# Kernel tuning notes

Measured on AMD Instinct MI355X. Metric: run time of the kernel, lower is better.

## Reference

```python
import jax, jax.numpy as jnp
from jax import lax
import numpy as np
import math

INPUT_DIM = 64
HIDDEN_DIM = 512
SEQ_LEN = 256
BATCH = 512
PRED_LEN = 24
NUM_TARGETS = 1


def setup_inputs() -> dict:
    key = jax.random.key(0)
    ks = jax.random.split(key, 10)
    stdv = 1.0 / math.sqrt(HIDDEN_DIM)
    u = lambda k, shape: jax.random.uniform(k, shape, jnp.float32, -stdv, stdv)
    return {
        "x": jax.random.normal(ks[0], (BATCH, SEQ_LEN, INPUT_DIM), jnp.float32),
        "Wa": u(ks[1], (INPUT_DIM, INPUT_DIM)),
        "Ua": u(ks[2], (2 * HIDDEN_DIM, INPUT_DIM)),
        "ba": jnp.zeros((INPUT_DIM,), jnp.float32),
        "Va": u(ks[3], (INPUT_DIM, INPUT_DIM)),
        "W_ih": u(ks[4], (4 * HIDDEN_DIM, INPUT_DIM)),
        "W_hh": u(ks[5], (4 * HIDDEN_DIM, HIDDEN_DIM)),
        "b_ih": u(ks[6], (4 * HIDDEN_DIM,)),
        "b_hh": u(ks[7], (4 * HIDDEN_DIM,)),
        "fc_w": u(ks[8], (PRED_LEN * NUM_TARGETS, HIDDEN_DIM)),
        "fc_b": u(ks[9], (PRED_LEN * NUM_TARGETS,)),
    }


def reference(x, Wa, Ua, ba, Va, W_ih, W_hh, b_ih, b_hh, fc_w, fc_b):
    B, S, D = x.shape
    H = W_hh.shape[1]

    def step(carry, x_t):
        h, c = carry  # [B,H] each
        # attention gate over input features
        hc = jnp.concatenate([h, c], axis=1)  # [B,2H]
        a_t = jnp.tanh(x_t @ Wa + hc @ Ua + ba) @ Va  # [B,D]
        alpha_t = jax.nn.softmax(a_t, axis=1)
        x_att = alpha_t * x_t
        # torch.nn.LSTMCell: gates in order i, f, g, o
        gates = x_att @ W_ih.T + h @ W_hh.T + b_ih + b_hh  # [B,4H]
        i, f, g, o = jnp.split(gates, 4, axis=1)
        c_new = jax.nn.sigmoid(f) * c + jax.nn.sigmoid(i) * jnp.tanh(g)
        h_new = jax.nn.sigmoid(o) * jnp.tanh(c_new)
        return (h_new, c_new), None

    h0 = jnp.zeros((B, H), x.dtype)
    c0 = jnp.zeros((B, H), x.dtype)
    (h_T, _), _ = lax.scan(step, (h0, c0), jnp.swapaxes(x, 0, 1))  # scan over seq
    y = h_T @ fc_w.T + fc_b  # [B, pred_len*num_targets]
    return y.reshape(B, PRED_LEN, NUM_TARGETS)
```

## Files before the change

kernel.cpp:

```cpp
#include <hip/hip_runtime.h>
#include <math.h>

#define B 512
#define S 256
#define D 64
#define H 512
#define BH (B*H)

#define HBUF_OFF 0
#define CBUF_OFF (2*BH)
#define XATT_OFF (4*BH)

typedef __attribute__((ext_vector_type(8))) short short8;
typedef __attribute__((ext_vector_type(4))) float f32x4;

__device__ inline unsigned short f2bf(float v) {
    unsigned int u = __float_as_uint(v);
    unsigned int r = (u + 0x7fffu + ((u >> 16) & 1u)) >> 16;
    return (unsigned short)r;
}
__device__ inline float bf2f(unsigned short b) {
    return __uint_as_float(((unsigned int)b) << 16);
}
__device__ inline float readlane_f(float v, int l) {
    return __uint_as_float(__builtin_amdgcn_readlane(__float_as_uint(v), l));
}

__global__ __launch_bounds__(256) void init_zero(float* __restrict__ ws) {
    int i = blockIdx.x * blockDim.x + threadIdx.x;
    if (i < BH) {
        ws[HBUF_OFF + i] = 0.f;
        ws[CBUF_OFF + i] = 0.f;
    }
}

__global__ __launch_bounds__(256) void attn_kernel(
    const float* __restrict__ x, const float* __restrict__ Wa,
    const float* __restrict__ Ua, const float* __restrict__ ba,
    const float* __restrict__ Va, float* __restrict__ ws, int t)
{
    const int tid = threadIdx.x;
    const int lane = tid & 63;
    const int w = tid >> 6;
    const int b0 = blockIdx.x * 4;
    const int rd = t & 1;

    __shared__ float hcx[4][1092];
    __shared__ float part[4][4][64];
    __shared__ float ta4[4][64];

    const float* __restrict__ hbuf = ws + HBUF_OFF + rd*BH;
    const float* __restrict__ cbuf = ws + CBUF_OFF + rd*BH;

    {
        const float4* xs = (const float4*)(x + ((size_t)(b0 + w)*S + t)*D);
        const float4* hs = (const float4*)(hbuf + (size_t)(b0 + w)*H);
        const float4* cs = (const float4*)(cbuf + (size_t)(b0 + w)*H);
        for (int c = lane; c < 272; c += 64) {
            float4 v;
            if (c < 16) v = xs[c];
            else if (c < 144) v = hs[c - 16];
            else v = cs[c - 144];
            *(float4*)&hcx[w][c*4] = v;
        }
    }
    __syncthreads();

    float acc0 = 0.f, acc1 = 0.f, acc2 = 0.f, acc3 = 0.f;
    const int k0 = w * 272;
    for (int kb = 0; kb < 272; kb += 64) {
        const int base = k0 + kb;
        int n = 272 - kb; if (n > 64) n = 64;
        int ii = base + lane; if (ii > 1087) ii = 1087;
        float hv0 = hcx[0][ii];
        float hv1 = hcx[1][ii];
        float hv2 = hcx[2][ii];
        float hv3 = hcx[3][ii];
        #pragma unroll 8
        for (int j = 0; j < n; ++j) {
            const int k = base + j;
            const float* wrow = (k < 64) ? (Wa + k*D) : (Ua + (size_t)(k - 64)*D);
            float uv = wrow[lane];
            acc0 += readlane_f(hv0, j) * uv;
            acc1 += readlane_f(hv1, j) * uv;
            acc2 += readlane_f(hv2, j) * uv;
            acc3 += readlane_f(hv3, j) * uv;
        }
    }
    part[w][0][lane] = acc0;
    part[w][1][lane] = acc1;
    part[w][2][lane] = acc2;
    part[w][3][lane] = acc3;
    __syncthreads();
    {
        float pre = ba[lane] + part[0][w][lane] + part[1][w][lane]
                  + part[2][w][lane] + part[3][w][lane];
        ta4[w][lane] = tanhf(pre);
    }
    __syncthreads();
    {
        float tv = ta4[w][lane];
        float v = 0.f;
        #pragma unroll 8
        for (int j = 0; j < 64; ++j)
            v += readlane_f(tv, j) * Va[j*D + lane];
        float m = v;
        #pragma unroll
        for (int o = 32; o > 0; o >>= 1) m = fmaxf(m, __shfl_xor(m, o));
        float e = expf(v - m);
        float ssum = e;
        #pragma unroll
        for (int o = 32; o > 0; o >>= 1) ssum += __shfl_xor(ssum, o);
        ws[XATT_OFF + (size_t)(b0 + w)*D + lane] = (e / ssum) * hcx[w][lane];
    }
}

__global__ __launch_bounds__(256) void gates_kernel(
    const float* __restrict__ Wih, const float* __restrict__ Whh,
    const float* __restrict__ bih, const float* __restrict__ bhh,
    float* __restrict__ ws, int t)
{
    const int tid = threadIdx.x;
    const int lane = tid & 63;
    const int wid = tid >> 6;
    const int wr = wid >> 1, wc = wid & 1;
    const int ut = blockIdx.x;
    const int rt = blockIdx.y;
    const int b0 = rt * 64;
    const int u_base = ut * 16;

    __shared__ __align__(16) unsigned short aHi[64][72];
    __shared__ __align__(16) unsigned short aLo[64][72];
    __shared__ __align__(16) unsigned short bHi[64][72];
    __shared__ __align__(16) unsigned short bLo[64][72];
    __shared__ float gout[64][66];

    const int rd = t & 1, wrs = rd ^ 1;
    const float* __restrict__ hbuf_r = ws + HBUF_OFF + rd*BH;
    const float* __restrict__ cbuf_r = ws + CBUF_OFF + rd*BH;
    float* __restrict__ hbuf_w = ws + HBUF_OFF + wrs*BH;
    float* __restrict__ cbuf_w = ws + CBUF_OFF + wrs*BH;
    const float* __restrict__ xatt = ws + XATT_OFF;

    const int srow = tid >> 2;
    const int c4 = tid & 3;
    const int Wrow = (srow & 3)*H + u_base + (srow >> 2);

    f32x4 acc00 = {0,0,0,0}, acc01 = {0,0,0,0}, acc10 = {0,0,0,0}, acc11 = {0,0,0,0};
    float4 aReg[4], bReg[4];

    auto loadChunk = [&](int kb) {
        const float* asrc; const float* bsrc;
        if (kb < 8) {
            asrc = hbuf_r + (size_t)(b0 + srow)*H + kb*64;
            bsrc = Whh + (size_t)Wrow*H + kb*64;
        } else {
            asrc = xatt + (size_t)(b0 + srow)*D;
            bsrc = Wih + (size_t)Wrow*D;
        }
        #pragma unroll
        for (int it = 0; it < 4; ++it) {
            const int f = c4 + 4*it;
            aReg[it] = *(const float4*)(asrc + f*4);
            bReg[it] = *(const float4*)(bsrc + f*4);
        }
    };
    auto storeChunk = [&]() {
        #pragma unroll
        for (int it = 0; it < 4; ++it) {
            const int f = c4 + 4*it;
            float4 av = aReg[it], bv = bReg[it];
            ushort4 ah, al, bh, bl;
            ah.x = f2bf(av.x); al.x = f2bf(av.x - bf2f(ah.x));
            ah.y = f2bf(av.y); al.y = f2bf(av.y - bf2f(ah.y));
            ah.z = f2bf(av.z); al.z = f2bf(av.z - bf2f(ah.z));
            ah.w = f2bf(av.w); al.w = f2bf(av.w - bf2f(ah.w));
            bh.x = f2bf(bv.x); bl.x = f2bf(bv.x - bf2f(bh.x));
            bh.y = f2bf(bv.y); bl.y = f2bf(bv.y - bf2f(bh.y));
            bh.z = f2bf(bv.z); bl.z = f2bf(bv.z - bf2f(bh.z));
            bh.w = f2bf(bv.w); bl.w = f2bf(bv.w - bf2f(bh.w));
            *(ushort4*)&aHi[srow][f*4] = ah;
            *(ushort4*)&aLo[srow][f*4] = al;
            *(ushort4*)&bHi[srow][f*4] = bh;
            *(ushort4*)&bLo[srow][f*4] = bl;
        }
    };

    loadChunk(0);
    for (int kb = 0; kb < 9; ++kb) {
        __syncthreads();
        storeChunk();
        __syncthreads();
        if (kb < 8) loadChunk(kb + 1);
        #pragma unroll
        for (int ks = 0; ks < 2; ++ks) {
            const int col = ks*32 + (lane >> 4)*8;
            const int ar0 = wr*32 + (lane & 15);
            const int br0 = wc*32 + (lane & 15);
            short8 ah0 = *(const short8*)&aHi[ar0][col];
            short8 ah1 = *(const short8*)&aHi[ar0 + 16][col];
            short8 al0 = *(const short8*)&aLo[ar0][col];
            short8 al1 = *(const short8*)&aLo[ar0 + 16][col];
            short8 bh0 = *(const short8*)&bHi[br0][col];
            short8 bh1 = *(const short8*)&bHi[br0 + 16][col];
            short8 bl0 = *(const short8*)&bLo[br0][col];
            short8 bl1 = *(const short8*)&bLo[br0 + 16][col];
            acc00 = __builtin_amdgcn_mfma_f32_16x16x32_bf16(ah0, bh0, acc00, 0,0,0);
            acc01 = __builtin_amdgcn_mfma_f32_16x16x32_bf16(ah0, bh1, acc01, 0,0,0);
            acc10 = __builtin_amdgcn_mfma_f32_16x16x32_bf16(ah1, bh0, acc10, 0,0,0);
            acc11 = __builtin_amdgcn_mfma_f32_16x16x32_bf16(ah1, bh1, acc11, 0,0,0);
            acc00 = __builtin_amdgcn_mfma_f32_16x16x32_bf16(ah0, bl0, acc00, 0,0,0);
            acc01 = __builtin_amdgcn_mfma_f32_16x16x32_bf16(ah0, bl1, acc01, 0,0,0);
            acc10 = __builtin_amdgcn_mfma_f32_16x16x32_bf16(ah1, bl0, acc10, 0,0,0);
            acc11 = __builtin_amdgcn_mfma_f32_16x16x32_bf16(ah1, bl1, acc11, 0,0,0);
            acc00 = __builtin_amdgcn_mfma_f32_16x16x32_bf16(al0, bh0, acc00, 0,0,0);
            acc01 = __builtin_amdgcn_mfma_f32_16x16x32_bf16(al0, bh1, acc01, 0,0,0);
            acc10 = __builtin_amdgcn_mfma_f32_16x16x32_bf16(al1, bh0, acc10, 0,0,0);
            acc11 = __builtin_amdgcn_mfma_f32_16x16x32_bf16(al1, bh1, acc11, 0,0,0);
        }
    }

    {
        const int m0 = (lane >> 4)*4;
        const int n0 = lane & 15;
        #pragma unroll
        for (int r = 0; r < 4; ++r) {
            gout[wr*32 + m0 + r     ][wc*32 + n0     ] = acc00[r];
            gout[wr*32 + m0 + r     ][wc*32 + 16 + n0] = acc01[r];
            gout[wr*32 + 16 + m0 + r][wc*32 + n0     ] = acc10[r];
            gout[wr*32 + 16 + m0 + r][wc*32 + 16 + n0] = acc11[r];
        }
    }
    __syncthreads();
    {
        const int u16 = tid & 15;
        const int u_glob = u_base + u16;
        const float bs0 = bih[0*H + u_glob] + bhh[0*H + u_glob];
        const float bs1 = bih[1*H + u_glob] + bhh[1*H + u_glob];
        const float bs2 = bih[2*H + u_glob] + bhh[2*H + u_glob];
        const float bs3 = bih[3*H + u_glob] + bhh[3*H + u_glob];
        #pragma unroll
        for (int pass = 0; pass < 4; ++pass) {
            const int b_loc = (tid >> 4) + pass*16;
            const int b = b0 + b_loc;
            float2 g01 = *(const float2*)&gout[b_loc][u16*4];
            float2 g23 = *(const float2*)&gout[b_loc][u16*4 + 2];
            float gi = g01.x + bs0;
            float gf = g01.y + bs1;
            float gg = g23.x + bs2;
            float go = g23.y + bs3;
            float c_old = cbuf_r[(size_t)b*H + u_glob];
            float si = 1.f/(1.f + expf(-gi));
            float sf = 1.f/(1.f + expf(-gf));
            float so = 1.f/(1.f + expf(-go));
            float cn = sf*c_old + si*tanhf(gg);
            float hn = so*tanhf(cn);
            cbuf_w[(size_t)b*H + u_glob] = cn;
            hbuf_w[(size_t)b*H + u_glob] = hn;
        }
    }
}

__global__ __launch_bounds__(256) void fc_kernel(
    const float* __restrict__ fcw, const float* __restrict__ fcb,
    const float* __restrict__ ws, float* __restrict__ out)
{
    const int b = blockIdx.x;
    __shared__ float hrow[H];
    const float* __restrict__ hp = ws + HBUF_OFF + (size_t)b*H;
    for (int k = threadIdx.x; k < H; k += 256) hrow[k] = hp[k];
    __syncthreads();
    int j = threadIdx.x;
    if (j < 24) {
        float a = fcb[j];
        #pragma unroll 8
        for (int k = 0; k < H; ++k) a += hrow[k] * fcw[j*H + k];
        out[b*24 + j] = a;
    }
}

extern "C" void kernel_launch(void* const* d_in, const int* in_sizes, int n_in,
                              void* d_out, int out_size, void* d_ws, size_t ws_size,
                              hipStream_t stream) {
    const float* x   = (const float*)d_in[0];
    const float* Wa  = (const float*)d_in[1];
    const float* Ua  = (const float*)d_in[2];
    const float* ba  = (const float*)d_in[3];
    const float* Va  = (const float*)d_in[4];
    const float* Wih = (const float*)d_in[5];
    const float* Whh = (const float*)d_in[6];
    const float* bih = (const float*)d_in[7];
    const float* bhh = (const float*)d_in[8];
    const float* fcw = (const float*)d_in[9];
    const float* fcb = (const float*)d_in[10];
    float* out = (float*)d_out;
    float* ws  = (float*)d_ws;

    hipLaunchKernelGGL(init_zero, dim3((BH + 255)/256), dim3(256), 0, stream, ws);
    for (int t = 0; t < S; ++t) {
        hipLaunchKernelGGL(attn_kernel, dim3(B/4), dim3(256), 0, stream,
                           x, Wa, Ua, ba, Va, ws, t);
        hipLaunchKernelGGL(gates_kernel, dim3(32, 8), dim3(256), 0, stream,
                           Wih, Whh, bih, bhh, ws, t);
    }
    hipLaunchKernelGGL(fc_kernel, dim3(B), dim3(256), 0, stream, fcw, fcb, ws, out);
}
```

Baseline: 9.084 ms.

## Pre-split weights into swizzled bf16 hi/lo and double-buffer the gates GEMM

A one-time prep kernel converts W_hh and W_ih into bf16 hi/lo pairs in a swizzled layout, so the gates kernel loads its B fragments straight into registers instead of converting them through LDS at every timestep. The gates kernel also writes h as bf16 hi/lo, and the attention kernel writes x_att the same way, so the A operand is staged into double-buffered LDS with a single barrier per k-chunk. The attention kernel is rewritten to handle two batch rows per block, reading h, c and weights directly from global memory. That rewrite gives up the four-row weight reuse of the old readlane scheme and may cost more in the attention step. The c state now uses one in-place buffer.

```diff
diff --git a/kernel.cpp b/kernel.cpp
--- a/kernel.cpp
+++ b/kernel.cpp
@@ -7,9 +7,6 @@
 #define H 512
 #define BH (B*H)
 
-#define HBUF_OFF 0
-#define CBUF_OFF (2*BH)
-#define XATT_OFF (4*BH)
 
 typedef __attribute__((ext_vector_type(8))) short short8;
 typedef __attribute__((ext_vector_type(4))) float f32x4;
@@ -22,103 +19,125 @@
 __device__ inline float bf2f(unsigned short b) {
     return __uint_as_float(((unsigned int)b) << 16);
 }
-__device__ inline float readlane_f(float v, int l) {
-    return __uint_as_float(__builtin_amdgcn_readlane(__float_as_uint(v), l));
-}
-
-__global__ __launch_bounds__(256) void init_zero(float* __restrict__ ws) {
+
+__global__ __launch_bounds__(256) void init_zero(
+    float* __restrict__ h32, float* __restrict__ c32,
+    unsigned short* __restrict__ hHi, unsigned short* __restrict__ hLo)
+{
     int i = blockIdx.x * blockDim.x + threadIdx.x;
     if (i < BH) {
-        ws[HBUF_OFF + i] = 0.f;
-        ws[CBUF_OFF + i] = 0.f;
+        h32[i] = 0.f;
+        c32[i] = 0.f;
+        hHi[i] = 0;
+        hLo[i] = 0;
+    }
+}
+
+__global__ __launch_bounds__(256) void prep_weights(
+    const float* __restrict__ Whh, const float* __restrict__ Wih,
+    unsigned short* __restrict__ wswz)
+{
+    const int ut = blockIdx.x;
+    const int kb = blockIdx.y;
+    const int t = threadIdx.x;
+    const int srow = t >> 2;
+    const int cc0 = (t & 3) * 16;
+    const int Wrow = (srow & 3)*H + ut*16 + (srow >> 2);
+
+    const float* src = (kb < 8) ? (Whh + (size_t)Wrow*H + kb*64 + cc0)
+                                : (Wih + (size_t)Wrow*D + cc0);
+    float v[16];
+    #pragma unroll
+    for (int i = 0; i < 4; ++i)
+        *(float4*)&v[i*4] = *(const float4*)(src + i*4);
+
+    unsigned short hi[16], lo[16];
+    #pragma unroll
+    for (int e = 0; e < 16; ++e) {
+        hi[e] = f2bf(v[e]);
+        lo[e] = f2bf(v[e] - bf2f(hi[e]));
+    }
+    #pragma unroll
+    for (int g = 0; g < 2; ++g) {
+        const int cc = cc0 + g*8;
+        const int ks = cc >> 5;
+        const int cg = (cc >> 3) & 3;
+        size_t bh = ((((size_t)(ut*9 + kb)*2 + 0)*2 + ks)*64 + srow)*32 + cg*8;
+        size_t bl = ((((size_t)(ut*9 + kb)*2 + 1)*2 + ks)*64 + srow)*32 + cg*8;
+        *(short8*)(wswz + bh) = *(const short8*)&hi[g*8];
+        *(short8*)(wswz + bl) = *(const short8*)&lo[g*8];
     }
 }
 
 __global__ __launch_bounds__(256) void attn_kernel(
     const float* __restrict__ x, const float* __restrict__ Wa,
     const float* __restrict__ Ua, const float* __restrict__ ba,
-    const float* __restrict__ Va, float* __restrict__ ws, int t)
-{
-    const int tid = threadIdx.x;
-    const int lane = tid & 63;
-    const int w = tid >> 6;
-    const int b0 = blockIdx.x * 4;
+    const float* __restrict__ Va,
+    const float* __restrict__ h32, const float* __restrict__ c32,
+    unsigned short* __restrict__ xHi, unsigned short* __restrict__ xLo, int t)
+{
+    const int d = threadIdx.x & 63;
+    const int r = (threadIdx.x >> 6) & 1;
+    const int p = threadIdx.x >> 7;
+    const int b = blockIdx.x * 2 + r;
+
     const int rd = t & 1;
-
-    __shared__ float hcx[4][1092];
-    __shared__ float part[4][4][64];
-    __shared__ float ta4[4][64];
-
-    const float* __restrict__ hbuf = ws + HBUF_OFF + rd*BH;
-    const float* __restrict__ cbuf = ws + CBUF_OFF + rd*BH;
-
+    const float* __restrict__ hrow = h32 + (size_t)rd*BH + (size_t)b*H;
+    const float* __restrict__ crow = c32 + (size_t)b*H;
+    const float* __restrict__ xrow = x + ((size_t)b*S + t)*D;
+
+    __shared__ float part[2][2][64];
+    __shared__ float ta[2][64];
+    __shared__ float pv[2][2][64];
+
+    float a = 0.f;
+    if (p == 0) {
+        a = ba[d];
+        #pragma unroll 8
+        for (int k = 0; k < D; ++k) a += xrow[k] * Wa[k*D + d];
+        #pragma unroll 8
+        for (int k = 0; k < H; ++k) a += hrow[k] * Ua[k*D + d];
+    } else {
+        #pragma unroll 8
+        for (int k = 0; k < H; ++k) a += crow[k] * Ua[(size_t)(H + k)*D + d];
+    }
+    part[r][p][d] = a;
+    __syncthreads();
+    if (p == 0) {
+        ta[r][d] = tanhf(part[r][0][d] + part[r][1][d]);
+    }
+    __syncthreads();
+    float av = 0.f;
     {
-        const float4* xs = (const float4*)(x + ((size_t)(b0 + w)*S + t)*D);
-        const float4* hs = (const float4*)(hbuf + (size_t)(b0 + w)*H);
-        const float4* cs = (const float4*)(cbuf + (size_t)(b0 + w)*H);
-        for (int c = lane; c < 272; c += 64) {
-            float4 v;
-            if (c < 16) v = xs[c];
-            else if (c < 144) v = hs[c - 16];
-            else v = cs[c - 144];
-            *(float4*)&hcx[w][c*4] = v;
-        }
-    }
-    __syncthreads();
-
-    float acc0 = 0.f, acc1 = 0.f, acc2 = 0.f, acc3 = 0.f;
-    const int k0 = w * 272;
-    for (int kb = 0; kb < 272; kb += 64) {
-        const int base = k0 + kb;
-        int n = 272 - kb; if (n > 64) n = 64;
-        int ii = base + lane; if (ii > 1087) ii = 1087;
-        float hv0 = hcx[0][ii];
-        float hv1 = hcx[1][ii];
-        float hv2 = hcx[2][ii];
-        float hv3 = hcx[3][ii];
-        #pragma unroll 8
-        for (int j = 0; j < n; ++j) {
-            const int k = base + j;
-            const float* wrow = (k < 64) ? (Wa + k*D) : (Ua + (size_t)(k - 64)*D);
-            float uv = wrow[lane];
-            acc0 += readlane_f(hv0, j) * uv;
-            acc1 += readlane_f(hv1, j) * uv;
-            acc2 += readlane_f(hv2, j) * uv;
-            acc3 += readlane_f(hv3, j) * uv;
-        }
-    }
-    part[w][0][lane] = acc0;
-    part[w][1][lane] = acc1;
-    part[w][2][lane] = acc2;
-    part[w][3][lane] = acc3;
-    __syncthreads();
-    {
-        float pre = ba[lane] + part[0][w][lane] + part[1][w][lane]
-                  + part[2][w][lane] + part[3][w][lane];
-        ta4[w][lane] = tanhf(pre);
-    }
-    __syncthreads();
-    {
-        float tv = ta4[w][lane];
-        float v = 0.f;
-        #pragma unroll 8
-        for (int j = 0; j < 64; ++j)
-            v += readlane_f(tv, j) * Va[j*D + lane];
-        float m = v;
-        #pragma unroll
-        for (int o = 32; o > 0; o >>= 1) m = fmaxf(m, __shfl_xor(m, o));
-        float e = expf(v - m);
-        float ssum = e;
-        #pragma unroll
-        for (int o = 32; o > 0; o >>= 1) ssum += __shfl_xor(ssum, o);
-        ws[XATT_OFF + (size_t)(b0 + w)*D + lane] = (e / ssum) * hcx[w][lane];
+        const int k0 = p * 32;
+        #pragma unroll 8
+        for (int k = k0; k < k0 + 32; ++k) av += ta[r][k] * Va[k*D + d];
+    }
+    pv[r][p][d] = av;
+    __syncthreads();
+    float v = pv[r][0][d] + pv[r][1][d];
+    float m = v;
+    #pragma unroll
+    for (int o = 32; o > 0; o >>= 1) m = fmaxf(m, __shfl_xor(m, o));
+    float e = expf(v - m);
+    float ssum = e;
+    #pragma unroll
+    for (int o = 32; o > 0; o >>= 1) ssum += __shfl_xor(ssum, o);
+    if (p == 0) {
+        float val = (e / ssum) * xrow[d];
+        unsigned short hi = f2bf(val);
+        unsigned short lo = f2bf(val - bf2f(hi));
+        xHi[(size_t)b*D + d] = hi;
+        xLo[(size_t)b*D + d] = lo;
     }
 }
 
 __global__ __launch_bounds__(256) void gates_kernel(
-    const float* __restrict__ Wih, const float* __restrict__ Whh,
-    const float* __restrict__ bih, const float* __restrict__ bhh,
-    float* __restrict__ ws, int t)
+    const unsigned short* __restrict__ wswz,
+    const unsigned short* __restrict__ hHi, const unsigned short* __restrict__ hLo,
+    const unsigned short* __restrict__ xHi, const unsigned short* __restrict__ xLo,
+    float* __restrict__ h32, float* __restrict__ c32,
+    const float* __restrict__ bih, const float* __restrict__ bhh, int t)
 {
     const int tid = threadIdx.x;
     const int lane = tid & 63;
@@ -128,83 +147,73 @@
     const int rt = blockIdx.y;
     const int b0 = rt * 64;
     const int u_base = ut * 16;
-
-    __shared__ __align__(16) unsigned short aHi[64][72];
-    __shared__ __align__(16) unsigned short aLo[64][72];
-    __shared__ __align__(16) unsigned short bHi[64][72];
-    __shared__ __align__(16) unsigned short bLo[64][72];
+    const int l15 = lane & 15;
+    const int cg = lane >> 4;
+
+    __shared__ __align__(16) unsigned short aHi[2][64][72];
+    __shared__ __align__(16) unsigned short aLo[2][64][72];
     __shared__ float gout[64][66];
 
     const int rd = t & 1, wrs = rd ^ 1;
-    const float* __restrict__ hbuf_r = ws + HBUF_OFF + rd*BH;
-    const float* __restrict__ cbuf_r = ws + CBUF_OFF + rd*BH;
-    float* __restrict__ hbuf_w = ws + HBUF_OFF + wrs*BH;
-    float* __restrict__ cbuf_w = ws + CBUF_OFF + wrs*BH;
-    const float* __restrict__ xatt = ws + XATT_OFF;
+    const unsigned short* __restrict__ hHiR = hHi + (size_t)rd*BH;
+    const unsigned short* __restrict__ hLoR = hLo + (size_t)rd*BH;
+
+    f32x4 acc00 = {0,0,0,0}, acc01 = {0,0,0,0}, acc10 = {0,0,0,0}, acc11 = {0,0,0,0};
+    short8 bre[2][2][2][2];
 
     const int srow = tid >> 2;
-    const int c4 = tid & 3;
-    const int Wrow = (srow & 3)*H + u_base + (srow >> 2);
-
-    f32x4 acc00 = {0,0,0,0}, acc01 = {0,0,0,0}, acc10 = {0,0,0,0}, acc11 = {0,0,0,0};
-    float4 aReg[4], bReg[4];
-
-    auto loadChunk = [&](int kb) {
-        const float* asrc; const float* bsrc;
+    const int q4 = tid & 3;
+
+    auto stageA = [&](int kb, int buf) {
+        const unsigned short *sh, *sl;
         if (kb < 8) {
-            asrc = hbuf_r + (size_t)(b0 + srow)*H + kb*64;
-            bsrc = Whh + (size_t)Wrow*H + kb*64;
+            size_t base = (size_t)(b0 + srow)*H + kb*64 + q4*16;
+            sh = hHiR + base; sl = hLoR + base;
         } else {
-            asrc = xatt + (size_t)(b0 + srow)*D;
-            bsrc = Wih + (size_t)Wrow*D;
-        }
+            size_t base = (size_t)(b0 + srow)*D + q4*16;
+            sh = xHi + base; sl = xLo + base;
+        }
+        *(short8*)&aHi[buf][srow][q4*16]     = *(const short8*)sh;
+        *(short8*)&aHi[buf][srow][q4*16 + 8] = *(const short8*)(sh + 8);
+        *(short8*)&aLo[buf][srow][q4*16]     = *(const short8*)sl;
+        *(short8*)&aLo[buf][srow][q4*16 + 8] = *(const short8*)(sl + 8);
+    };
+    auto loadB = [&](int kb, int set) {
         #pragma unroll
-        for (int it = 0; it < 4; ++it) {
-            const int f = c4 + 4*it;
-            aReg[it] = *(const float4*)(asrc + f*4);
-            bReg[it] = *(const float4*)(bsrc + f*4);
-        }
+        for (int half = 0; half < 2; ++half)
+            #pragma unroll
+            for (int ks = 0; ks < 2; ++ks)
+                #pragma unroll
+                for (int rb = 0; rb < 2; ++rb) {
+                    const unsigned short* p = wswz +
+                        ((((size_t)(ut*9 + kb)*2 + half)*2 + ks)*64
+                         + wc*32 + rb*16 + l15)*32 + cg*8;
+                    bre[set][half][ks][rb] = *(const short8*)p;
+                }
     };
-    auto storeChunk = [&]() {
-        #pragma unroll
-        for (int it = 0; it < 4; ++it) {
-            const int f = c4 + 4*it;
-            float4 av = aReg[it], bv = bReg[it];
-            ushort4 ah, al, bh, bl;
-            ah.x = f2bf(av.x); al.x = f2bf(av.x - bf2f(ah.x));
-            ah.y = f2bf(av.y); al.y = f2bf(av.y - bf2f(ah.y));
-            ah.z = f2bf(av.z); al.z = f2bf(av.z - bf2f(ah.z));
-            ah.w = f2bf(av.w); al.w = f2bf(av.w - bf2f(ah.w));
-            bh.x = f2bf(bv.x); bl.x = f2bf(bv.x - bf2f(bh.x));
-            bh.y = f2bf(bv.y); bl.y = f2bf(bv.y - bf2f(bh.y));
-            bh.z = f2bf(bv.z); bl.z = f2bf(bv.z - bf2f(bh.z));
-            bh.w = f2bf(bv.w); bl.w = f2bf(bv.w - bf2f(bh.w));
-            *(ushort4*)&aHi[srow][f*4] = ah;
-            *(ushort4*)&aLo[srow][f*4] = al;
-            *(ushort4*)&bHi[srow][f*4] = bh;
-            *(ushort4*)&bLo[srow][f*4] = bl;
-        }
-    };
-
-    loadChunk(0);
+
+    stageA(0, 0);
+    loadB(0, 0);
+    __syncthreads();
+
+    #pragma unroll
     for (int kb = 0; kb < 9; ++kb) {
-        __syncthreads();
-        storeChunk();
-        __syncthreads();
-        if (kb < 8) loadChunk(kb + 1);
+        const int cur = kb & 1;
+        if (kb < 8) {
+            stageA(kb + 1, cur ^ 1);
+            loadB(kb + 1, cur ^ 1);
+        }
         #pragma unroll
         for (int ks = 0; ks < 2; ++ks) {
-            const int col = ks*32 + (lane >> 4)*8;
-            const int ar0 = wr*32 + (lane & 15);
-            const int br0 = wc*32 + (lane & 15);
-            short8 ah0 = *(const short8*)&aHi[ar0][col];
-            short8 ah1 = *(const short8*)&aHi[ar0 + 16][col];
-            short8 al0 = *(const short8*)&aLo[ar0][col];
-            short8 al1 = *(const short8*)&aLo[ar0 + 16][col];
-            short8 bh0 = *(const short8*)&bHi[br0][col];
-            short8 bh1 = *(const short8*)&bHi[br0 + 16][col];
-            short8 bl0 = *(const short8*)&bLo[br0][col];
-            short8 bl1 = *(const short8*)&bLo[br0 + 16][col];
+            const int col = ks*32 + cg*8;
+            short8 ah0 = *(const short8*)&aHi[cur][wr*32 + l15][col];
+            short8 ah1 = *(const short8*)&aHi[cur][wr*32 + 16 + l15][col];
+            short8 al0 = *(const short8*)&aLo[cur][wr*32 + l15][col];
+            short8 al1 = *(const short8*)&aLo[cur][wr*32 + 16 + l15][col];
+            short8 bh0 = bre[cur][0][ks][0];
+            short8 bh1 = bre[cur][0][ks][1];
+            short8 bl0 = bre[cur][1][ks][0];
+            short8 bl1 = bre[cur][1][ks][1];
             acc00 = __builtin_amdgcn_mfma_f32_16x16x32_bf16(ah0, bh0, acc00, 0,0,0);
             acc01 = __builtin_amdgcn_mfma_f32_16x16x32_bf16(ah0, bh1, acc01, 0,0,0);
             acc10 = __builtin_amdgcn_mfma_f32_16x16x32_bf16(ah1, bh0, acc10, 0,0,0);
@@ -218,10 +227,11 @@
             acc10 = __builtin_amdgcn_mfma_f32_16x16x32_bf16(al1, bh0, acc10, 0,0,0);
             acc11 = __builtin_amdgcn_mfma_f32_16x16x32_bf16(al1, bh1, acc11, 0,0,0);
         }
+        __syncthreads();
     }
 
     {
-        const int m0 = (lane >> 4)*4;
+        const int m0 = (lane >> 4) * 4;
         const int n0 = lane & 15;
         #pragma unroll
         for (int r = 0; r < 4; ++r) {
@@ -239,6 +249,9 @@
         const float bs1 = bih[1*H + u_glob] + bhh[1*H + u_glob];
         const float bs2 = bih[2*H + u_glob] + bhh[2*H + u_glob];
         const float bs3 = bih[3*H + u_glob] + bhh[3*H + u_glob];
+        float* __restrict__ h32w = h32 + (size_t)wrs*BH;
+        unsigned short* __restrict__ hHiW = (unsigned short*)hHi + (size_t)wrs*BH;
+        unsigned short* __restrict__ hLoW = (unsigned short*)hLo + (size_t)wrs*BH;
         #pragma unroll
         for (int pass = 0; pass < 4; ++pass) {
             const int b_loc = (tid >> 4) + pass*16;
@@ -249,25 +262,30 @@
             float gf = g01.y + bs1;
             float gg = g23.x + bs2;
             float go = g23.y + bs3;
-            float c_old = cbuf_r[(size_t)b*H + u_glob];
+            const size_t idx = (size_t)b*H + u_glob;
+            float c_old = c32[idx];
             float si = 1.f/(1.f + expf(-gi));
             float sf = 1.f/(1.f + expf(-gf));
             float so = 1.f/(1.f + expf(-go));
             float cn = sf*c_old + si*tanhf(gg);
             float hn = so*tanhf(cn);
-            cbuf_w[(size_t)b*H + u_glob] = cn;
-            hbuf_w[(size_t)b*H + u_glob] = hn;
+            c32[idx] = cn;
+            h32w[idx] = hn;
+            unsigned short hi = f2bf(hn);
+            unsigned short lo = f2bf(hn - bf2f(hi));
+            hHiW[idx] = hi;
+            hLoW[idx] = lo;
         }
     }
 }
 
 __global__ __launch_bounds__(256) void fc_kernel(
     const float* __restrict__ fcw, const float* __restrict__ fcb,
-    const float* __restrict__ ws, float* __restrict__ out)
+    const float* __restrict__ h32, float* __restrict__ out)
 {
     const int b = blockIdx.x;
     __shared__ float hrow[H];
-    const float* __restrict__ hp = ws + HBUF_OFF + (size_t)b*H;
+    const float* __restrict__ hp = h32 + (size_t)b*H;
     for (int k = threadIdx.x; k < H; k += 256) hrow[k] = hp[k];
     __syncthreads();
     int j = threadIdx.x;
@@ -294,14 +312,25 @@
     const float* fcw = (const float*)d_in[9];
     const float* fcb = (const float*)d_in[10];
     float* out = (float*)d_out;
-    float* ws  = (float*)d_ws;
-
-    hipLaunchKernelGGL(init_zero, dim3((BH + 255)/256), dim3(256), 0, stream, ws);
+
+    char* base = (char*)d_ws;
+    float* h32 = (float*)(base);
+    float* c32 = (float*)(base + (size_t)2*BH*4);
+    unsigned short* hHi = (unsigned short*)(base + (size_t)3*BH*4);
+    unsigned short* hLo = hHi + (size_t)2*BH;
+    unsigned short* xHi = hLo + (size_t)2*BH;
+    unsigned short* xLo = xHi + (size_t)B*D;
+    unsigned short* wswz = xLo + (size_t)B*D;
+
+    hipLaunchKernelGGL(init_zero, dim3((BH + 255)/256), dim3(256), 0, stream,
+                       h32, c32, hHi, hLo);
+    hipLaunchKernelGGL(prep_weights, dim3(32, 9), dim3(256), 0, stream,
+                       Whh, Wih, wswz);
     for (int t = 0; t < S; ++t) {
-        hipLaunchKernelGGL(attn_kernel, dim3(B/4), dim3(256), 0, stream,
-                           x, Wa, Ua, ba, Va, ws, t);
+        hipLaunchKernelGGL(attn_kernel, dim3(B/2), dim3(256), 0, stream,
+                           x, Wa, Ua, ba, Va, h32, c32, xHi, xLo, t);
         hipLaunchKernelGGL(gates_kernel, dim3(32, 8), dim3(256), 0, stream,
-                           Wih, Whh, bih, bhh, ws, t);
-    }
-    hipLaunchKernelGGL(fc_kernel, dim3(B), dim3(256), 0, stream, fcw, fcb, ws, out);
-}
+                           wswz, hHi, hLo, xHi, xLo, h32, c32, bih, bhh, t);
+    }
+    hipLaunchKernelGGL(fc_kernel, dim3(B), dim3(256), 0, stream, fcw, fcb, h32, out);
+}
```

Result: faster. 8.384 ms (-7.7%).
